# Kernel optimization log

Measured on AMD Instinct MI355X. Metric: run time of the kernel, lower is better.

## Reference

```python
import jax, jax.numpy as jnp
import numpy as np

K = 1024   # number of NNLS components (theta_1 is K x K)
B = 8192   # batched frames / columns


def setup_inputs() -> dict:
    key = jax.random.key(0)
    k1, k2, k3, k4 = jax.random.split(key, 4)
    # theta_1 = I - AtA / ||AtA||_F  -> near-identity contraction; emulate with
    # identity minus a small random symmetric-ish perturbation.
    pert = jax.random.normal(k1, (K, K), dtype=jnp.float32) * (1.0 / K)
    th1 = jnp.eye(K, dtype=jnp.float32) - pert
    Y = jax.random.uniform(k2, (K, B), dtype=jnp.float32)
    X_old = jax.random.uniform(k3, (K, B), dtype=jnp.float32)
    weight = jax.random.normal(k4, (K, B), dtype=jnp.float32) * 0.1  # theta_2 = Atb/n_AtA
    k = 2  # PGD iteration counter
    return {"th1": th1, "Y": Y, "X_old": X_old, "k": k, "weight": weight}


def reference(th1, Y, X_old, k, weight):
    # One projected-gradient-descent step of NNLS with Nesterov momentum:
    #   new_X = relu(th1 @ Y + weight)
    #   Y_new = new_X + (k-1)/(k+2) * (new_X - X_old)
    kf = jnp.float32(k)
    new_X = jax.nn.relu(jnp.matmul(th1, Y) + weight)          # [K, B]
    momentum = (kf - 1.0) / (kf + 2.0)
    Y_new = new_X + momentum * (new_X - X_old)                # [K, B]
    return (Y_new, new_X, k + 1, weight)
```

## Files before the change

kernel.cpp:

```cpp
#include <hip/hip_runtime.h>
#include <cstdint>


#define KDIM 1024
#define NDIM 8192
#define KB_ELEMS (1024UL * 8192UL)
#define YT_BYTES (8192UL * 1024UL * 2UL)
#define AB_BYTES (1024UL * 1024UL * 2UL)
#define WS_NEED (YT_BYTES + AB_BYTES)

typedef short short8 __attribute__((ext_vector_type(8)));
typedef float f32x4 __attribute__((ext_vector_type(4)));

struct __attribute__((aligned(4))) f4u { float x, y, z, w; };

__device__ __forceinline__ uint32_t pk2(float a, float b) {
  uint32_t ua = __builtin_bit_cast(uint32_t, a) + 0x8000u;
  uint32_t ub = __builtin_bit_cast(uint32_t, b) + 0x8000u;
  return (ua >> 16) | (ub & 0xFFFF0000u);
}

__device__ __forceinline__ void ldsload16(const void* g, void* l) {
  __builtin_amdgcn_global_load_lds(
      (const __attribute__((address_space(1))) uint32_t*)g,
      (__attribute__((address_space(3))) uint32_t*)l, 16, 0, 0);
}

__global__ __launch_bounds__(256) void nnls_conv(
    const float* __restrict__ th1, const float* __restrict__ Y,
    char* __restrict__ ws)
{
  unsigned short* yt  = (unsigned short*)ws;
  unsigned short* abf = (unsigned short*)(ws + YT_BYTES);
  const int tid = threadIdx.x;
  if (blockIdx.x < 512) {
    const int kt = blockIdx.x >> 4;
    const int n  = (blockIdx.x & 15) * 512 + tid * 2;
    const float* src = Y + (size_t)kt * 32 * NDIM + n;
    float2 v[32];
#pragma unroll
    for (int r = 0; r < 32; ++r) v[r] = *(const float2*)&src[(size_t)r * NDIM];
    __attribute__((aligned(16))) uint32_t oA[16], oB[16];
#pragma unroll
    for (int r = 0; r < 16; ++r) {
      oA[r] = pk2(v[2 * r].x, v[2 * r + 1].x);
      oB[r] = pk2(v[2 * r].y, v[2 * r + 1].y);
    }
    const int perm = (n >> 1) & 3;
    uint4* dst = (uint4*)(yt + ((size_t)kt * NDIM + n) * 32);
    const uint4* a4 = (const uint4*)oA;
    const uint4* b4 = (const uint4*)oB;
#pragma unroll
    for (int q = 0; q < 4; ++q) dst[q ^ perm] = a4[q];
#pragma unroll
    for (int q = 0; q < 4; ++q) dst[4 + (q ^ perm)] = b4[q];
  } else {
    const int id = (blockIdx.x - 512) * 256 + tid;
    const int kt = id >> 10, m = id & 1023;
    const float4* s4 = (const float4*)(th1 + (size_t)m * KDIM + kt * 32);
    __attribute__((aligned(16))) uint32_t o[16];
#pragma unroll
    for (int q = 0; q < 8; ++q) {
      const float4 v = s4[q];
      o[2 * q]     = pk2(v.x, v.y);
      o[2 * q + 1] = pk2(v.z, v.w);
    }
    const int perm = (m >> 1) & 3;
    uint4* dst = (uint4*)(abf + ((size_t)kt * KDIM + m) * 32);
    const uint4* o4 = (const uint4*)o;
#pragma unroll
    for (int q = 0; q < 4; ++q) dst[q ^ perm] = o4[q];
  }
}

__global__ __launch_bounds__(128, 2) void nnls_gemm4(
    const char* __restrict__ ws, const float* __restrict__ xold,
    const int* __restrict__ kin, const float* __restrict__ weight,
    float* __restrict__ out)
{
  const char* yt = ws;
  const char* ab = ws + YT_BYTES;
  __shared__ __align__(16) char smem[36864];

  const int tid  = threadIdx.x;
  const int lane = tid & 63;
  const int w    = tid >> 6;
  const int quad = lane >> 4, nl = lane & 15;

  const int m0 = blockIdx.y * 128;
  const int n0 = blockIdx.x * 64;

  const char* ag = ab + (size_t)m0 * 64 + w * 4096 + lane * 16;
  const char* bg = yt + (size_t)n0 * 64 + w * 2048 + lane * 16;

  auto stage = [&](int kt, int buf) {
    const char* a2 = ag + (size_t)kt * 65536;
    const char* b2 = bg + (size_t)kt * 524288;
    char* d = smem + buf * 12288;
#pragma unroll
    for (int q = 0; q < 4; ++q) ldsload16(a2 + q * 1024, d + w * 4096 + q * 1024);
#pragma unroll
    for (int q = 0; q < 2; ++q) ldsload16(b2 + q * 1024, d + 8192 + w * 2048 + q * 1024);
  };

  stage(0, 0);
  stage(1, 1);

  f32x4 acc[4][4] = {};
  const int fro = (quad ^ ((nl >> 1) & 3)) * 8;

#pragma unroll
  for (int kt = 0; kt < 32; ++kt) {
    if (kt == 31) { asm volatile("s_waitcnt vmcnt(0)" ::: "memory"); }
    else          { asm volatile("s_waitcnt vmcnt(6)" ::: "memory"); }
    __builtin_amdgcn_s_barrier();
    if (kt < 30) stage(kt + 2, (kt + 2) % 3);

    const unsigned short* Asp = (const unsigned short*)(smem + (kt % 3) * 12288);
    const unsigned short* Bsp = Asp + 4096;
    short8 af[4], bf[4];
#pragma unroll
    for (int i = 0; i < 4; ++i)
      af[i] = *(const short8*)&Asp[(w * 64 + i * 16 + nl) * 32 + fro];
#pragma unroll
    for (int j = 0; j < 4; ++j)
      bf[j] = *(const short8*)&Bsp[(j * 16 + nl) * 32 + fro];
#pragma unroll
    for (int i = 0; i < 4; ++i)
#pragma unroll
      for (int j = 0; j < 4; ++j)
        acc[i][j] = __builtin_amdgcn_mfma_f32_16x16x32_bf16(af[i], bf[j], acc[i][j], 0, 0, 0);
  }

  const float kf  = (float)kin[0];
  const float mom = (kf - 1.0f) / (kf + 2.0f);
  float* ep = (float*)(smem + w * 4608);
  const int u  = lane >> 4;
  const int cq = lane & 15;

#pragma unroll
  for (int i = 0; i < 4; ++i) {
    const int mgb = m0 + w * 64 + i * 16;
    size_t idxs[4]; float4 wv[4], xo[4];
#pragma unroll
    for (int t = 0; t < 4; ++t) {
      idxs[t] = (size_t)(mgb + t * 4 + u) * NDIM + n0 + cq * 4;
      wv[t] = *(const float4*)&weight[idxs[t]];
      xo[t] = *(const float4*)&xold[idxs[t]];
    }
#pragma unroll
    for (int j = 0; j < 4; ++j)
#pragma unroll
      for (int r = 0; r < 4; ++r)
        ep[(quad * 4 + r) * 68 + j * 16 + nl] = acc[i][j][r];
#pragma unroll
    for (int t = 0; t < 4; ++t) {
      const float4 cv = *(const float4*)&ep[(t * 4 + u) * 68 + cq * 4];
      const size_t idx = idxs[t];
      float4 nx, yn;
      nx.x = fmaxf(cv.x + wv[t].x, 0.0f); nx.y = fmaxf(cv.y + wv[t].y, 0.0f);
      nx.z = fmaxf(cv.z + wv[t].z, 0.0f); nx.w = fmaxf(cv.w + wv[t].w, 0.0f);
      yn.x = nx.x + mom * (nx.x - xo[t].x); yn.y = nx.y + mom * (nx.y - xo[t].y);
      yn.z = nx.z + mom * (nx.z - xo[t].z); yn.w = nx.w + mom * (nx.w - xo[t].w);
      *(float4*)&out[idx] = yn;
      *(float4*)&out[KB_ELEMS + idx] = nx;
      f4u s; s.x = wv[t].x; s.y = wv[t].y; s.z = wv[t].z; s.w = wv[t].w;
      *(f4u*)&out[2 * KB_ELEMS + 1 + idx] = s;
    }
  }

  if (blockIdx.x == 0 && blockIdx.y == 0 && tid == 0)
    out[2 * KB_ELEMS] = (float)(kin[0] + 1);
}

#define LDA 40
__global__ __launch_bounds__(512, 4) void nnls_gemm_v1(
    const float* __restrict__ th1, const float* __restrict__ Y,
    const float* __restrict__ xold, const int* __restrict__ kin,
    const float* __restrict__ weight, float* __restrict__ out)
{
  __shared__ __align__(16) char smem[40960];
  unsigned short* As0 = (unsigned short*)smem;
  unsigned short* Bs0 = (unsigned short*)(smem + 10240);
  unsigned short* As1 = (unsigned short*)(smem + 20480);
  unsigned short* Bs1 = (unsigned short*)(smem + 30720);

  const int tid  = threadIdx.x;
  const int lane = tid & 63;
  const int w    = tid >> 6;
  const int wm = w >> 1, wn = w & 1;
  const int quad = lane >> 4, nl = lane & 15;
  const int m0 = blockIdx.y * 128;
  const int n0 = blockIdx.x * 128;
  const int ar = tid >> 3;
  const int ac = tid & 7;
  const float* abase = th1 + (size_t)(m0 + ar) * KDIM + ac * 4;
  const int bn = tid & 127;
  const int bk = (tid >> 7) * 8;
  const float* ybase = Y + (size_t)bk * NDIM + n0 + bn;

  float4 abv[2];
  float  yb[8];
  abv[0] = *(const float4*)(abase);
  abv[1] = *(const float4*)(abase + (size_t)64 * KDIM);
#pragma unroll
  for (int r = 0; r < 8; ++r) yb[r] = ybase[(size_t)r * NDIM];

  f32x4 acc[2][4] = {};

#pragma unroll 2
  for (int kt = 0; kt < 32; ++kt) {
    unsigned short* Asp = (kt & 1) ? As1 : As0;
    unsigned short* Bsp = (kt & 1) ? Bs1 : Bs0;
    {
      uint2 d0; d0.x = pk2(abv[0].x, abv[0].y); d0.y = pk2(abv[0].z, abv[0].w);
      *(uint2*)&Asp[ar * LDA + ac * 4] = d0;
      uint2 d1; d1.x = pk2(abv[1].x, abv[1].y); d1.y = pk2(abv[1].z, abv[1].w);
      *(uint2*)&Asp[(ar + 64) * LDA + ac * 4] = d1;
      uint4 e;
      e.x = pk2(yb[0], yb[1]); e.y = pk2(yb[2], yb[3]);
      e.z = pk2(yb[4], yb[5]); e.w = pk2(yb[6], yb[7]);
      *(uint4*)&Bsp[bn * LDA + bk] = e;
    }
    __syncthreads();
    if (kt < 31) {
      const float* an = abase + (kt + 1) * 32;
      abv[0] = *(const float4*)(an);
      abv[1] = *(const float4*)(an + (size_t)64 * KDIM);
      const float* yn = ybase + (size_t)((kt + 1) * 32) * NDIM;
#pragma unroll
      for (int r = 0; r < 8; ++r) yb[r] = yn[(size_t)r * NDIM];
    }
    short8 af[2], bf[4];
#pragma unroll
    for (int i = 0; i < 2; ++i)
      af[i] = *(const short8*)&Asp[(wm * 32 + i * 16 + nl) * LDA + quad * 8];
#pragma unroll
    for (int j = 0; j < 4; ++j)
      bf[j] = *(const short8*)&Bsp[(wn * 64 + j * 16 + nl) * LDA + quad * 8];
#pragma unroll
    for (int i = 0; i < 2; ++i)
#pragma unroll
      for (int j = 0; j < 4; ++j)
        acc[i][j] = __builtin_amdgcn_mfma_f32_16x16x32_bf16(af[i], bf[j], acc[i][j], 0, 0, 0);
    __syncthreads();
  }
  __syncthreads();

  const float kf  = (float)kin[0];
  const float mom = (kf - 1.0f) / (kf + 2.0f);
  float* ep = (float*)smem + w * 1088;
  const int u  = lane >> 4;
  const int mc = lane & 15;
#pragma unroll
  for (int i = 0; i < 2; ++i) {
#pragma unroll
    for (int j = 0; j < 4; ++j)
#pragma unroll
      for (int r = 0; r < 4; ++r)
        ep[(quad * 4 + r) * 68 + (j * 16 + nl)] = acc[i][j][r];
    const int mgb = m0 + wm * 32 + i * 16;
#pragma unroll
    for (int t = 0; t < 4; ++t) {
      const int row = t * 4 + u;
      const float4 cv = *(const float4*)&ep[row * 68 + mc * 4];
      const int ng = n0 + wn * 64 + mc * 4;
      const size_t idx = (size_t)(mgb + row) * NDIM + ng;
      const float4 wv = *(const float4*)&weight[idx];
      const float4 xo = *(const float4*)&xold[idx];
      float4 nx, yn;
      nx.x = fmaxf(cv.x + wv.x, 0.0f); nx.y = fmaxf(cv.y + wv.y, 0.0f);
      nx.z = fmaxf(cv.z + wv.z, 0.0f); nx.w = fmaxf(cv.w + wv.w, 0.0f);
      yn.x = nx.x + mom * (nx.x - xo.x); yn.y = nx.y + mom * (nx.y - xo.y);
      yn.z = nx.z + mom * (nx.z - xo.z); yn.w = nx.w + mom * (nx.w - xo.w);
      *(float4*)&out[idx] = yn;
      *(float4*)&out[KB_ELEMS + idx] = nx;
      f4u s; s.x = wv.x; s.y = wv.y; s.z = wv.z; s.w = wv.w;
      *(f4u*)&out[2 * KB_ELEMS + 1 + idx] = s;
    }
  }
  if (blockIdx.x == 0 && blockIdx.y == 0 && tid == 0)
    out[2 * KB_ELEMS] = (float)(kin[0] + 1);
}

extern "C" void kernel_launch(void* const* d_in, const int* in_sizes, int n_in,
                              void* d_out, int out_size, void* d_ws, size_t ws_size,
                              hipStream_t stream) {
  const float* th1  = (const float*)d_in[0];
  const float* Y    = (const float*)d_in[1];
  const float* xold = (const float*)d_in[2];
  const int*   kin  = (const int*)d_in[3];
  const float* wgt  = (const float*)d_in[4];
  float* out = (float*)d_out;

  if (d_ws != nullptr && ws_size >= WS_NEED) {
    nnls_conv<<<640, 256, 0, stream>>>(th1, Y, (char*)d_ws);
    nnls_gemm4<<<dim3(NDIM / 64, KDIM / 128), 128, 0, stream>>>(
        (const char*)d_ws, xold, kin, wgt, out);
  } else {
    nnls_gemm_v1<<<dim3(NDIM / 128, KDIM / 128), 512, 0, stream>>>(
        th1, Y, xold, kin, wgt, out);
  }
}
```

Baseline: 233.7 us.

## Split GEMM tile across four waves and narrow Y conversion threads

The GEMM kernel now runs the same 128x64 output tile with four waves in a 2x2 arrangement instead of two waves, so each wave holds a 64x32 accumulator. Each wave also issues fewer async global-to-LDS loads per stage, and the launch bounds allow more resident waves. The Y bf16 conversion kernel now gives each thread one column instead of two and uses twice as many blocks. The aim is more latency hiding through higher occupancy, at the cost of more LDS fragment reads per MFMA, since the A fragments are loaded by two waves each.

```diff
diff --git a/kernel.cpp b/kernel.cpp
--- a/kernel.cpp
+++ b/kernel.cpp
@@ -33,29 +33,23 @@
   unsigned short* yt  = (unsigned short*)ws;
   unsigned short* abf = (unsigned short*)(ws + YT_BYTES);
   const int tid = threadIdx.x;
-  if (blockIdx.x < 512) {
-    const int kt = blockIdx.x >> 4;
-    const int n  = (blockIdx.x & 15) * 512 + tid * 2;
+  if (blockIdx.x < 1024) {
+    const int kt = blockIdx.x >> 5;
+    const int n  = (blockIdx.x & 31) * 256 + tid;
     const float* src = Y + (size_t)kt * 32 * NDIM + n;
-    float2 v[32];
-#pragma unroll
-    for (int r = 0; r < 32; ++r) v[r] = *(const float2*)&src[(size_t)r * NDIM];
-    __attribute__((aligned(16))) uint32_t oA[16], oB[16];
-#pragma unroll
-    for (int r = 0; r < 16; ++r) {
-      oA[r] = pk2(v[2 * r].x, v[2 * r + 1].x);
-      oB[r] = pk2(v[2 * r].y, v[2 * r + 1].y);
-    }
+    float v[32];
+#pragma unroll
+    for (int r = 0; r < 32; ++r) v[r] = src[(size_t)r * NDIM];
+    __attribute__((aligned(16))) uint32_t o[16];
+#pragma unroll
+    for (int r = 0; r < 16; ++r) o[r] = pk2(v[2 * r], v[2 * r + 1]);
     const int perm = (n >> 1) & 3;
     uint4* dst = (uint4*)(yt + ((size_t)kt * NDIM + n) * 32);
-    const uint4* a4 = (const uint4*)oA;
-    const uint4* b4 = (const uint4*)oB;
-#pragma unroll
-    for (int q = 0; q < 4; ++q) dst[q ^ perm] = a4[q];
-#pragma unroll
-    for (int q = 0; q < 4; ++q) dst[4 + (q ^ perm)] = b4[q];
+    const uint4* o4 = (const uint4*)o;
+#pragma unroll
+    for (int q = 0; q < 4; ++q) dst[q ^ perm] = o4[q];
   } else {
-    const int id = (blockIdx.x - 512) * 256 + tid;
+    const int id = (blockIdx.x - 1024) * 256 + tid;
     const int kt = id >> 10, m = id & 1023;
     const float4* s4 = (const float4*)(th1 + (size_t)m * KDIM + kt * 32);
     __attribute__((aligned(16))) uint32_t o[16];
@@ -73,7 +67,7 @@
   }
 }
 
-__global__ __launch_bounds__(128, 2) void nnls_gemm4(
+__global__ __launch_bounds__(256, 4) void nnls_gemm5(
     const char* __restrict__ ws, const float* __restrict__ xold,
     const int* __restrict__ kin, const float* __restrict__ weight,
     float* __restrict__ out)
@@ -85,77 +79,77 @@
   const int tid  = threadIdx.x;
   const int lane = tid & 63;
   const int w    = tid >> 6;
+  const int wm = w >> 1, wn = w & 1;
   const int quad = lane >> 4, nl = lane & 15;
 
   const int m0 = blockIdx.y * 128;
   const int n0 = blockIdx.x * 64;
 
-  const char* ag = ab + (size_t)m0 * 64 + w * 4096 + lane * 16;
-  const char* bg = yt + (size_t)n0 * 64 + w * 2048 + lane * 16;
+  const char* ag = ab + (size_t)m0 * 64 + w * 1024 + lane * 16;
+  const char* bg = yt + (size_t)n0 * 64 + w * 1024 + lane * 16;
 
   auto stage = [&](int kt, int buf) {
     const char* a2 = ag + (size_t)kt * 65536;
     const char* b2 = bg + (size_t)kt * 524288;
     char* d = smem + buf * 12288;
-#pragma unroll
-    for (int q = 0; q < 4; ++q) ldsload16(a2 + q * 1024, d + w * 4096 + q * 1024);
-#pragma unroll
-    for (int q = 0; q < 2; ++q) ldsload16(b2 + q * 1024, d + 8192 + w * 2048 + q * 1024);
+    ldsload16(a2,        d + w * 1024);
+    ldsload16(a2 + 4096, d + 4096 + w * 1024);
+    ldsload16(b2,        d + 8192 + w * 1024);
   };
 
   stage(0, 0);
   stage(1, 1);
 
-  f32x4 acc[4][4] = {};
+  f32x4 acc[4][2] = {};
   const int fro = (quad ^ ((nl >> 1) & 3)) * 8;
 
 #pragma unroll
   for (int kt = 0; kt < 32; ++kt) {
     if (kt == 31) { asm volatile("s_waitcnt vmcnt(0)" ::: "memory"); }
-    else          { asm volatile("s_waitcnt vmcnt(6)" ::: "memory"); }
+    else          { asm volatile("s_waitcnt vmcnt(3)" ::: "memory"); }
     __builtin_amdgcn_s_barrier();
     if (kt < 30) stage(kt + 2, (kt + 2) % 3);
 
     const unsigned short* Asp = (const unsigned short*)(smem + (kt % 3) * 12288);
     const unsigned short* Bsp = Asp + 4096;
-    short8 af[4], bf[4];
+    short8 af[4], bf[2];
 #pragma unroll
     for (int i = 0; i < 4; ++i)
-      af[i] = *(const short8*)&Asp[(w * 64 + i * 16 + nl) * 32 + fro];
-#pragma unroll
-    for (int j = 0; j < 4; ++j)
-      bf[j] = *(const short8*)&Bsp[(j * 16 + nl) * 32 + fro];
+      af[i] = *(const short8*)&Asp[(wm * 64 + i * 16 + nl) * 32 + fro];
+#pragma unroll
+    for (int j = 0; j < 2; ++j)
+      bf[j] = *(const short8*)&Bsp[(wn * 32 + j * 16 + nl) * 32 + fro];
 #pragma unroll
     for (int i = 0; i < 4; ++i)
 #pragma unroll
-      for (int j = 0; j < 4; ++j)
+      for (int j = 0; j < 2; ++j)
         acc[i][j] = __builtin_amdgcn_mfma_f32_16x16x32_bf16(af[i], bf[j], acc[i][j], 0, 0, 0);
   }
 
   const float kf  = (float)kin[0];
   const float mom = (kf - 1.0f) / (kf + 2.0f);
-  float* ep = (float*)(smem + w * 4608);
-  const int u  = lane >> 4;
-  const int cq = lane & 15;
+  float* ep = (float*)smem + w * 576;
+  const int rl = lane >> 3;
+  const int cc = lane & 7;
 
 #pragma unroll
   for (int i = 0; i < 4; ++i) {
-    const int mgb = m0 + w * 64 + i * 16;
-    size_t idxs[4]; float4 wv[4], xo[4];
-#pragma unroll
-    for (int t = 0; t < 4; ++t) {
-      idxs[t] = (size_t)(mgb + t * 4 + u) * NDIM + n0 + cq * 4;
+    const int mgb = m0 + wm * 64 + i * 16;
+    size_t idxs[2]; float4 wv[2], xo[2];
+#pragma unroll
+    for (int t = 0; t < 2; ++t) {
+      idxs[t] = (size_t)(mgb + t * 8 + rl) * NDIM + n0 + wn * 32 + cc * 4;
       wv[t] = *(const float4*)&weight[idxs[t]];
       xo[t] = *(const float4*)&xold[idxs[t]];
     }
 #pragma unroll
-    for (int j = 0; j < 4; ++j)
+    for (int j = 0; j < 2; ++j)
 #pragma unroll
       for (int r = 0; r < 4; ++r)
-        ep[(quad * 4 + r) * 68 + j * 16 + nl] = acc[i][j][r];
-#pragma unroll
-    for (int t = 0; t < 4; ++t) {
-      const float4 cv = *(const float4*)&ep[(t * 4 + u) * 68 + cq * 4];
+        ep[(quad * 4 + r) * 36 + j * 16 + nl] = acc[i][j][r];
+#pragma unroll
+    for (int t = 0; t < 2; ++t) {
+      const float4 cv = *(const float4*)&ep[(t * 8 + rl) * 36 + cc * 4];
       const size_t idx = idxs[t];
       float4 nx, yn;
       nx.x = fmaxf(cv.x + wv[t].x, 0.0f); nx.y = fmaxf(cv.y + wv[t].y, 0.0f);
@@ -294,8 +288,8 @@
   float* out = (float*)d_out;
 
   if (d_ws != nullptr && ws_size >= WS_NEED) {
-    nnls_conv<<<640, 256, 0, stream>>>(th1, Y, (char*)d_ws);
-    nnls_gemm4<<<dim3(NDIM / 64, KDIM / 128), 128, 0, stream>>>(
+    nnls_conv<<<1152, 256, 0, stream>>>(th1, Y, (char*)d_ws);
+    nnls_gemm5<<<dim3(NDIM / 64, KDIM / 128), 256, 0, stream>>>(
         (const char*)d_ws, xold, kin, wgt, out);
   } else {
     nnls_gemm_v1<<<dim3(NDIM / 128, KDIM / 128), 512, 0, stream>>>(
```

Result: faster. 225.7 us (-3.5%).
